# Performance work log

Measured on AMD Instinct MI355X. Metric: run time of the kernel, lower is better.

The kernel has to match this reference:

```python
import jax, jax.numpy as jnp
import numpy as np

H = 8        # n_attention_heads
D = 512      # model_dimension (full per-head dim in this module!)
DFF = 2048   # feed_forward_internal_dimension
B, T = 8, 1024
EPS = 1e-5


def _layernorm(x, g, b, eps=EPS):
    mu = jnp.mean(x, axis=-1, keepdims=True)
    var = jnp.mean(jnp.square(x - mu), axis=-1, keepdims=True)
    return (x - mu) * jax.lax.rsqrt(var + eps) * g + b


def setup_inputs() -> dict:
    key = jax.random.key(0)
    ks = jax.random.split(key, 16)
    s_d = 1.0 / np.sqrt(D)
    s_c = 1.0 / np.sqrt(H * D)
    s_f = 1.0 / np.sqrt(DFF)
    return {
        "x":   jax.random.normal(ks[0], (B, T, D), jnp.float32),
        # per-head projections, stored (in, out); stacked over heads
        "Wq":  jax.random.normal(ks[1], (H, D, D), jnp.float32) * s_d,
        "bq":  jax.random.normal(ks[2], (H, D), jnp.float32) * 0.02,
        "Wk":  jax.random.normal(ks[3], (H, D, D), jnp.float32) * s_d,
        "bk":  jax.random.normal(ks[4], (H, D), jnp.float32) * 0.02,
        "Wv":  jax.random.normal(ks[5], (H, D, D), jnp.float32) * s_d,
        "bv":  jax.random.normal(ks[6], (H, D), jnp.float32) * 0.02,
        "Wo":  jax.random.normal(ks[7], (H * D, D), jnp.float32) * s_c,
        "bo":  jax.random.normal(ks[8], (D,), jnp.float32) * 0.02,
        "ln1_g": 1.0 + 0.1 * jax.random.normal(ks[9], (D,), jnp.float32),
        "ln1_b": 0.1 * jax.random.normal(ks[10], (D,), jnp.float32),
        "W1":  jax.random.normal(ks[11], (D, DFF), jnp.float32) * s_d,
        "b1":  jax.random.normal(ks[12], (DFF,), jnp.float32) * 0.02,
        "W2":  jax.random.normal(ks[13], (DFF, D), jnp.float32) * s_f,
        "b2":  jax.random.normal(ks[14], (D,), jnp.float32) * 0.02,
        "ln2_g": 1.0 + 0.1 * jax.random.normal(ks[15], (D,), jnp.float32),
        "ln2_b": jnp.zeros((D,), jnp.float32),
    }


def reference(x, Wq, bq, Wk, bk, Wv, bv, Wo, bo, ln1_g, ln1_b,
              W1, b1, W2, b2, ln2_g, ln2_b):
    # --- multi-head attention (each head uses the FULL d_model) ---
    # q,k,v: [H, B, T, D]
    q = jnp.einsum("btd,hde->hbte", x, Wq) + bq[:, None, None, :]
    k = jnp.einsum("btd,hde->hbte", x, Wk) + bk[:, None, None, :]
    v = jnp.einsum("btd,hde->hbte", x, Wv) + bv[:, None, None, :]
    scores = jnp.einsum("hbte,hbse->hbts", q, k) * (D ** -0.5)  # [H,B,T,T]
    attn = jax.nn.softmax(scores, axis=-1)
    heads = jnp.einsum("hbts,hbse->hbte", attn, v)  # [H,B,T,D]
    # concat heads along features: [B,T,H*D]
    concat = jnp.transpose(heads, (1, 2, 0, 3)).reshape(x.shape[0], x.shape[1], -1)
    mha = concat @ Wo + bo
    # residual + LayerNorm (dropout_p = 0)
    y1 = _layernorm(mha + x, ln1_g, ln1_b)
    # --- FFN: note source applies ReLU AFTER the second Linear, then skip ---
    ff = jax.nn.relu((y1 @ W1 + b1) @ W2 + b2) + y1
    out = _layernorm(ff, ln2_g, ln2_b)
    return out
```

## Files before the change

kernel.cpp:

```cpp
#include <hip/hip_runtime.h>

using u16 = unsigned short;
using bf16x8 = __attribute__((ext_vector_type(8))) short;
using f32x4 = __attribute__((ext_vector_type(4))) float;

__device__ __forceinline__ u16 f2bf(float f) {
  unsigned x = __float_as_uint(f);
  x += 0x7fffu + ((x >> 16) & 1u);
  return (u16)(x >> 16);
}

__device__ __forceinline__ void gl2lds16(const u16* g, u16* l) {
  __builtin_amdgcn_global_load_lds(
      (const __attribute__((address_space(1))) unsigned int*)g,
      (__attribute__((address_space(3))) unsigned int*)l, 16, 0, 0);
}

__global__ __launch_bounds__(256) void cvt_all(
    const float* __restrict__ x, u16* __restrict__ Krep,
    const float* __restrict__ Wq, const float* __restrict__ Wk,
    const float* __restrict__ Wv, const float* __restrict__ Wo,
    const float* __restrict__ W1, const float* __restrict__ W2,
    u16* __restrict__ Wqb, u16* __restrict__ Wkb, u16* __restrict__ WvT,
    u16* __restrict__ WoT, u16* __restrict__ W1T, u16* __restrict__ W2T)
{
  int b = blockIdx.x, tid = threadIdx.x;
  if (b < 4096) {
    int i = b * 1024 + tid * 4;
    float4 v = *(const float4*)(x + i);
    ushort4 o;
    o.x = f2bf(v.x); o.y = f2bf(v.y); o.z = f2bf(v.z); o.w = f2bf(v.w);
    *(ushort4*)(Krep + i) = o;
    return;
  }
  if (b < 8192) {
    const float* s; u16* d; int i;
    if (b < 6144) { s = Wq; d = Wqb; i = (b - 4096) * 1024 + tid * 4; }
    else          { s = Wk; d = Wkb; i = (b - 6144) * 1024 + tid * 4; }
    float4 v = *(const float4*)(s + i);
    ushort4 o;
    o.x = f2bf(v.x); o.y = f2bf(v.y); o.z = f2bf(v.z); o.w = f2bf(v.w);
    *(ushort4*)(d + i) = o;
    return;
  }
  __shared__ float T[32][33];
  const float* s; u16* d; int K, N, k0, n0;
  int i = b - 8192;
  if (i < 2048) {
    int h = i / 256, tl = i % 256;
    s = Wv + (size_t)h * 262144; d = WvT + (size_t)h * 262144;
    K = 512; N = 512; n0 = (tl % 16) * 32; k0 = (tl / 16) * 32;
  } else if (i < 4096) {
    int j = i - 2048;
    s = Wo; d = WoT; K = 4096; N = 512; n0 = (j % 16) * 32; k0 = (j / 16) * 32;
  } else if (i < 5120) {
    int j = i - 4096;
    s = W1; d = W1T; K = 512; N = 2048; n0 = (j % 64) * 32; k0 = (j / 64) * 32;
  } else {
    int j = i - 5120;
    s = W2; d = W2T; K = 2048; N = 512; n0 = (j % 16) * 32; k0 = (j / 16) * 32;
  }
  int r = tid >> 3, c4 = (tid & 7) << 2;
  float4 v = *(const float4*)(s + (size_t)(k0 + r) * N + n0 + c4);
  T[r][c4 + 0] = v.x; T[r][c4 + 1] = v.y; T[r][c4 + 2] = v.z; T[r][c4 + 3] = v.w;
  __syncthreads();
  ushort4 o;
  o.x = f2bf(T[c4 + 0][r]); o.y = f2bf(T[c4 + 1][r]);
  o.z = f2bf(T[c4 + 2][r]); o.w = f2bf(T[c4 + 3][r]);
  *(ushort4*)(d + (size_t)(n0 + r) * K + k0 + c4) = o;
}

__global__ __launch_bounds__(256) void wk_bias(
    const float* __restrict__ Wk, const float* __restrict__ bq,
    float* __restrict__ wbuf)
{
  int r = blockIdx.x * 4 + (threadIdx.x >> 6);
  int lane = threadIdx.x & 63;
  int h = r >> 9, a = r & 511;
  const float* row = Wk + ((size_t)h * 512 + a) * 512 + lane * 8;
  const float* bqp = bq + h * 512 + lane * 8;
  float4 w0 = *(const float4*)row, w1 = *(const float4*)(row + 4);
  float4 b0 = *(const float4*)bqp, b1 = *(const float4*)(bqp + 4);
  float s = w0.x * b0.x + w0.y * b0.y + w0.z * b0.z + w0.w * b0.w +
            w1.x * b1.x + w1.y * b1.y + w1.z * b1.z + w1.w * b1.w;
  #pragma unroll
  for (int off = 1; off < 64; off <<= 1) s += __shfl_xor(s, off);
  if (lane == 0) wbuf[r] = s;
}

template<int BM>
__global__ __launch_bounds__(256) void gemm_bt(
    const u16* __restrict__ A, const u16* __restrict__ Bt,
    const float* __restrict__ bias, void* __restrict__ Cout,
    int M, int N, int K, int lda, int ldb, long long kzoff,
    long long sBz, long long sbz, long long sCzBytes, int out_mode)
{
  constexpr int MT = BM / 32;
  __shared__ __align__(16) u16 smem[BM * 32 + 128 * 32];
  u16* As = smem;
  u16* Bs = smem + BM * 32;
  const f32x4 zero4 = {0.f, 0.f, 0.f, 0.f};

  const u16* Ap = A + (size_t)blockIdx.z * (size_t)kzoff;
  const u16* Bp = Bt + (size_t)blockIdx.z * (size_t)(sBz + kzoff);
  const float* biasp = bias ? bias + (size_t)blockIdx.z * sbz : nullptr;
  char* Cp = (char*)Cout + (size_t)blockIdx.z * sCzBytes;

  int tid = threadIdx.x;
  int lane = tid & 63, wave = tid >> 6;
  int m = lane & 15, quad = lane >> 4;
  int wm = (wave >> 1) * (BM / 2), wn = (wave & 1) * 64;
  int m0 = blockIdx.y * BM, n0 = blockIdx.x * 128;
  int lr = lane >> 2, lc = (lane & 3) << 3;

  f32x4 acc[MT][4];
  #pragma unroll
  for (int i = 0; i < MT; i++)
    #pragma unroll
    for (int j = 0; j < 4; j++) acc[i][j] = zero4;

  for (int k0 = 0; k0 < K; k0 += 32) {
    #pragma unroll
    for (int i = 0; i < BM / 64; i++) {
      int rb = i * 64 + wave * 16;
      gl2lds16(Ap + (size_t)(m0 + rb + lr) * lda + k0 + lc, &As[rb * 32]);
    }
    #pragma unroll
    for (int i = 0; i < 2; i++) {
      int rb = i * 64 + wave * 16;
      gl2lds16(Bp + (size_t)(n0 + rb + lr) * ldb + k0 + lc, &Bs[rb * 32]);
    }
    __syncthreads();

    bf16x8 af[MT], bfr[4];
    #pragma unroll
    for (int t = 0; t < MT; t++)
      af[t] = *(const bf16x8*)&As[(wm + t * 16 + m) * 32 + quad * 8];
    #pragma unroll
    for (int t = 0; t < 4; t++)
      bfr[t] = *(const bf16x8*)&Bs[(wn + t * 16 + m) * 32 + quad * 8];
    #pragma unroll
    for (int mt = 0; mt < MT; mt++)
      #pragma unroll
      for (int nt = 0; nt < 4; nt++)
        acc[mt][nt] = __builtin_amdgcn_mfma_f32_16x16x32_bf16(af[mt], bfr[nt],
                                                              acc[mt][nt], 0, 0, 0);
    __syncthreads();
  }

  if (out_mode == 2) {
    u16* Ts = smem;
    int b2 = m0 >> 10, t20 = m0 & 1023;
    int half = wave >> 1;
    #pragma unroll
    for (int mt = 0; mt < MT; mt++) {
      #pragma unroll
      for (int nt = 0; nt < 4; nt++) {
        int colc = wn + nt * 16 + m;
        float bb = biasp ? biasp[n0 + colc] : 0.f;
        #pragma unroll
        for (int r = 0; r < 4; r++)
          Ts[colc * 40 + half * 16 + quad * 4 + r] = f2bf(acc[mt][nt][r] + bb);
      }
      __syncthreads();
      #pragma unroll
      for (int it = 0; it < 2; it++) {
        int c = (tid >> 2) + 64 * it;
        int j = tid & 3;
        bf16x8 v = *(const bf16x8*)&Ts[c * 40 + j * 8];
        int tg = t20 + (j >> 1) * (BM / 2) + mt * 16 + (j & 1) * 8;
        *(bf16x8*)((u16*)Cp + ((size_t)b2 * 512 + n0 + c) * 1024 + tg) = v;
      }
      __syncthreads();
    }
    return;
  }

  #pragma unroll
  for (int nt = 0; nt < 4; nt++) {
    int col = n0 + wn + nt * 16 + m;
    float bb = biasp ? biasp[col] : 0.f;
    #pragma unroll
    for (int mt = 0; mt < MT; mt++) {
      #pragma unroll
      for (int r = 0; r < 4; r++) {
        int row = m0 + wm + mt * 16 + quad * 4 + r;
        float v = acc[mt][nt][r] + bb;
        if (out_mode == 1) {
          ((u16*)Cp)[(size_t)row * N + col] = f2bf(v);
        } else {
          ((float*)Cp)[(size_t)row * N + col] = v;
        }
      }
    }
  }
}

__global__ __launch_bounds__(256) void gemm_tv16(
    const u16* __restrict__ A, const u16* __restrict__ Mt,
    const u16* __restrict__ WvT, const float* __restrict__ wbuf,
    const float* __restrict__ bv, u16* __restrict__ Tg, u16* __restrict__ Vg)
{
  __shared__ __align__(16) u16 smem[8192];
  u16* As = smem;
  u16* Bs = smem + 4096;
  const f32x4 zero4 = {0.f, 0.f, 0.f, 0.f};

  int z = blockIdx.z;
  int t = z >> 3, h = z & 7;
  const u16* Bp = (t == 0 ? Mt : WvT) + (size_t)h * 262144;
  const float* biasp = (t == 0 ? wbuf : bv) + h * 512;
  u16* Og = (t == 0 ? Tg : Vg) + (size_t)h * 4194304;

  int tid = threadIdx.x;
  int lane = tid & 63, wave = tid >> 6;
  int m = lane & 15, quad = lane >> 4;
  int wm = (wave >> 1) * 64, wn = (wave & 1) * 64;
  int m0 = blockIdx.y * 128, n0 = blockIdx.x * 128;
  int lr = lane >> 2, lc = (lane & 3) << 3;

  f32x4 acc[4][4];
  #pragma unroll
  for (int i = 0; i < 4; i++)
    #pragma unroll
    for (int j = 0; j < 4; j++) acc[i][j] = zero4;

  for (int k0 = 0; k0 < 512; k0 += 32) {
    #pragma unroll
    for (int i = 0; i < 2; i++) {
      int rb = i * 64 + wave * 16;
      gl2lds16(A + (size_t)(m0 + rb + lr) * 512 + k0 + lc, &As[rb * 32]);
      gl2lds16(Bp + (size_t)(n0 + rb + lr) * 512 + k0 + lc, &Bs[rb * 32]);
    }
    __syncthreads();
    bf16x8 af[4], bfr[4];
    #pragma unroll
    for (int tt = 0; tt < 4; tt++) {
      af[tt]  = *(const bf16x8*)&As[(wm + tt * 16 + m) * 32 + quad * 8];
      bfr[tt] = *(const bf16x8*)&Bs[(wn + tt * 16 + m) * 32 + quad * 8];
    }
    #pragma unroll
    for (int mt = 0; mt < 4; mt++)
      #pragma unroll
      for (int nt = 0; nt < 4; nt++)
        acc[mt][nt] = __builtin_amdgcn_mfma_f32_16x16x32_bf16(af[mt], bfr[nt],
                                                              acc[mt][nt], 0, 0, 0);
    __syncthreads();
  }

  if (t == 1) {
    u16* Ts = smem;
    int b2 = m0 >> 10, t20 = m0 & 1023;
    int half = wave >> 1;
    #pragma unroll
    for (int mt = 0; mt < 4; mt++) {
      #pragma unroll
      for (int nt = 0; nt < 4; nt++) {
        int colc = wn + nt * 16 + m;
        float bb = biasp[n0 + colc];
        #pragma unroll
        for (int r = 0; r < 4; r++)
          Ts[colc * 40 + half * 16 + quad * 4 + r] = f2bf(acc[mt][nt][r] + bb);
      }
      __syncthreads();
      #pragma unroll
      for (int it = 0; it < 2; it++) {
        int c = (tid >> 2) + 64 * it;
        int j = tid & 3;
        bf16x8 v = *(const bf16x8*)&Ts[c * 40 + j * 8];
        int tg = t20 + (j >> 1) * 64 + mt * 16 + (j & 1) * 8;
        *(bf16x8*)(Og + ((size_t)b2 * 512 + n0 + c) * 1024 + tg) = v;
      }
      __syncthreads();
    }
    return;
  }

  #pragma unroll
  for (int nt = 0; nt < 4; nt++) {
    int col = n0 + wn + nt * 16 + m;
    float bb = biasp[col];
    #pragma unroll
    for (int mt = 0; mt < 4; mt++) {
      #pragma unroll
      for (int r = 0; r < 4; r++) {
        int row = m0 + wm + mt * 16 + quad * 4 + r;
        Og[(size_t)row * 512 + col] = f2bf(acc[mt][nt][r] + bb);
      }
    }
  }
}

__global__ __launch_bounds__(256, 2) void attn_kernel(
    const u16* __restrict__ Tg, const u16* __restrict__ Krep,
    const u16* __restrict__ Vg, u16* __restrict__ Oc, int h0)
{
  __shared__ __align__(16) u16 Kt[32][520];
  __shared__ __align__(16) u16 Vt[512][32];
  __shared__ __align__(16) u16 Pl[4][16][40];
  const f32x4 zero4 = {0.f, 0.f, 0.f, 0.f};

  int b = blockIdx.x, qb = blockIdx.y, z = blockIdx.z;
  int h = h0 + z;

  size_t hb = ((size_t)z * 8 + b) * (size_t)(1024 * 512);
  const u16* Tp = Tg + hb;
  const u16* Kp = Krep + (size_t)b * (size_t)(1024 * 512);
  const u16* Vp = Vg + hb;

  int tid = threadIdx.x, lane = tid & 63, wave = tid >> 6;
  int m = lane & 15, quad = lane >> 4;
  int q0 = qb * 64 + wave * 16;

  bf16x8 aq[16];
  #pragma unroll
  for (int kc = 0; kc < 16; kc++)
    aq[kc] = *(const bf16x8*)(Tp + (size_t)(q0 + m) * 512 + kc * 32 + quad * 8);

  f32x4 acc[32];
  #pragma unroll
  for (int dt = 0; dt < 32; dt++) acc[dt] = zero4;
  f32x4 lsum = zero4;
  const float scale = 0.04419417382415922f;
  short one = 0x3F80;
  bf16x8 bones = {one, one, one, one, one, one, one, one};

  int vrow = lane >> 2;
  int vcol = (lane & 3) << 3;

  for (int kt = 0; kt < 32; kt++) {
    int kr0 = kt * 32;
    #pragma unroll
    for (int r = 0; r < 8; r++) {
      int row = wave * 8 + r;
      gl2lds16(Kp + (size_t)(kr0 + row) * 512 + lane * 8, &Kt[row][0]);
    }
    #pragma unroll
    for (int i = 0; i < 8; i++) {
      int j = wave * 8 + i;
      gl2lds16(Vp + (size_t)(j * 16 + vrow) * 1024 + kr0 + vcol, &Vt[j * 16][0]);
    }
    __syncthreads();

    f32x4 s0 = zero4, s1 = zero4;
    __builtin_amdgcn_s_setprio(1);
    #pragma unroll
    for (int kc = 0; kc < 16; kc++) {
      bf16x8 bk0 = *(const bf16x8*)&Kt[m][kc * 32 + quad * 8];
      bf16x8 bk1 = *(const bf16x8*)&Kt[m + 16][kc * 32 + quad * 8];
      s0 = __builtin_amdgcn_mfma_f32_16x16x32_bf16(aq[kc], bk0, s0, 0, 0, 0);
      s1 = __builtin_amdgcn_mfma_f32_16x16x32_bf16(aq[kc], bk1, s1, 0, 0, 0);
    }
    __builtin_amdgcn_s_setprio(0);

    #pragma unroll
    for (int r = 0; r < 4; r++) {
      Pl[wave][quad * 4 + r][m]      = f2bf(__expf(s0[r] * scale));
      Pl[wave][quad * 4 + r][m + 16] = f2bf(__expf(s1[r] * scale));
    }
    asm volatile("s_waitcnt lgkmcnt(0)" ::: "memory");
    bf16x8 ap = *(const bf16x8*)&Pl[wave][m][quad * 8];

    lsum = __builtin_amdgcn_mfma_f32_16x16x32_bf16(ap, bones, lsum, 0, 0, 0);

    __builtin_amdgcn_s_setprio(1);
    #pragma unroll
    for (int dt = 0; dt < 32; dt++) {
      bf16x8 bv = *(const bf16x8*)&Vt[dt * 16 + m][quad * 8];
      acc[dt] = __builtin_amdgcn_mfma_f32_16x16x32_bf16(ap, bv, acc[dt], 0, 0, 0);
    }
    __builtin_amdgcn_s_setprio(0);
    __syncthreads();
  }

  float linv[4];
  #pragma unroll
  for (int r = 0; r < 4; r++) linv[r] = 1.f / lsum[r];
  #pragma unroll
  for (int dt = 0; dt < 32; dt++) {
    #pragma unroll
    for (int r = 0; r < 4; r++) {
      size_t trow = (size_t)b * 1024 + q0 + quad * 4 + r;
      Oc[(trow * 8 + h) * 512 + dt * 16 + m] = f2bf(acc[dt][r] * linv[r]);
    }
  }
}

__global__ __launch_bounds__(256) void ln_kernel(
    const float* __restrict__ xin0, const float* __restrict__ xin1,
    const float* __restrict__ bias, const float* __restrict__ res,
    const float* __restrict__ gam, const float* __restrict__ bet,
    float* __restrict__ outf, u16* __restrict__ outb, int do_relu)
{
  __shared__ float red[4];
  __shared__ float red2[4];
  int row = blockIdx.x, t = threadIdx.x;
  size_t base = (size_t)row * 512;
  float a0 = xin0[base + t] + bias[t];
  float a1 = xin0[base + 256 + t] + bias[256 + t];
  if (xin1) { a0 += xin1[base + t]; a1 += xin1[base + 256 + t]; }
  if (do_relu) { a0 = fmaxf(a0, 0.f); a1 = fmaxf(a1, 0.f); }
  a0 += res[base + t]; a1 += res[base + 256 + t];

  float s = a0 + a1;
  #pragma unroll
  for (int off = 32; off > 0; off >>= 1) s += __shfl_xor(s, off);
  if ((t & 63) == 0) red[t >> 6] = s;
  __syncthreads();
  float mu = (red[0] + red[1] + red[2] + red[3]) * (1.f / 512.f);

  float d0 = a0 - mu, d1 = a1 - mu;
  float q = d0 * d0 + d1 * d1;
  #pragma unroll
  for (int off = 32; off > 0; off >>= 1) q += __shfl_xor(q, off);
  if ((t & 63) == 0) red2[t >> 6] = q;
  __syncthreads();
  float var = (red2[0] + red2[1] + red2[2] + red2[3]) * (1.f / 512.f);
  float rs = rsqrtf(var + 1e-5f);

  float o0 = d0 * rs * gam[t] + bet[t];
  float o1 = d1 * rs * gam[t + 256] + bet[t + 256];
  outf[base + t] = o0;
  outf[base + 256 + t] = o1;
  if (outb) { outb[base + t] = f2bf(o0); outb[base + 256 + t] = f2bf(o1); }
}

extern "C" void kernel_launch(void* const* d_in, const int* in_sizes, int n_in,
                              void* d_out, int out_size, void* d_ws, size_t ws_size,
                              hipStream_t stream) {
  const float* x   = (const float*)d_in[0];
  const float* Wq  = (const float*)d_in[1];
  const float* bq  = (const float*)d_in[2];
  const float* Wk  = (const float*)d_in[3];
  const float* bk  = (const float*)d_in[4];
  const float* Wv  = (const float*)d_in[5];
  const float* bv  = (const float*)d_in[6];
  const float* Wo  = (const float*)d_in[7];
  const float* bo  = (const float*)d_in[8];
  const float* g1  = (const float*)d_in[9];
  const float* bn1 = (const float*)d_in[10];
  const float* W1  = (const float*)d_in[11];
  const float* bf1 = (const float*)d_in[12];
  const float* W2  = (const float*)d_in[13];
  const float* bf2 = (const float*)d_in[14];
  const float* g2  = (const float*)d_in[15];
  const float* bn2 = (const float*)d_in[16];
  (void)bk;

  const size_t HB = 8388608;
  char* ws = (char*)d_ws;
  u16* Krep = (u16*)(ws + 0);
  u16* xb   = Krep;
  u16* Wqb = (u16*)(ws + 67108864);
  u16* Wkb = (u16*)(ws + 71303168);
  u16* WvT = (u16*)(ws + 75497472);
  u16* WoT = (u16*)(ws + 79691776);
  u16* W1T = (u16*)(ws + 83886080);
  u16* W2T = (u16*)(ws + 85983232);
  u16* Mt  = (u16*)(ws + 88080384);
  float* wbuf = (float*)(ws + 92274688);
  u16* cc  = (u16*)(ws + 92291072);
  size_t tvbase = 159399936;
  size_t G = 1;
  if (ws_size >= 293617664ULL) G = 8;
  else if (ws_size >= 226508800ULL) G = 4;
  else if (ws_size >= 218120192ULL) G = 2;
  u16* Tg = (u16*)(ws + tvbase);
  u16* Vg = (u16*)(ws + tvbase + G * HB);
  float* y1f  = (float*)(ws + 159399936);
  u16*   y1b  = (u16*)(ws + 176177152);
  float* mha0 = (float*)(ws + 184565760);
  float* mha1 = (float*)(ws + 201342976);
  u16*   ff1  = (u16*)(ws + 92291072);
  float* ff20 = (float*)(ws + 125845504);
  float* ff21 = (float*)(ws + 142622720);

  cvt_all<<<14336, 256, 0, stream>>>(x, Krep, Wq, Wk, Wv, Wo, W1, W2,
                                     Wqb, Wkb, WvT, WoT, W1T, W2T);
  gemm_bt<128><<<dim3(4, 4, 8), 256, 0, stream>>>(Wkb, Wqb, nullptr, Mt,
      512, 512, 512, 512, 512, 262144LL, 0LL, 0LL, 524288LL, 1);
  wk_bias<<<1024, 256, 0, stream>>>(Wk, bq, wbuf);

  dim3 blk(256);
  if (G == 8) {
    gemm_tv16<<<dim3(4, 64, 16), blk, 0, stream>>>(xb, Mt, WvT, wbuf, bv,
                                                   Tg, Vg);
    attn_kernel<<<dim3(8, 16, 8), 256, 0, stream>>>(Tg, Krep, Vg, cc, 0);
  } else {
    for (int h0 = 0; h0 < 8; h0 += (int)G) {
      dim3 gqkv(4, 64, (unsigned)G);
      gemm_bt<128><<<gqkv, blk, 0, stream>>>(xb, Mt + (size_t)h0 * 262144,
          wbuf + h0 * 512, Tg, 8192, 512, 512, 512, 512, 0LL,
          262144LL, 512LL, (long long)HB, 1);
      gemm_bt<128><<<gqkv, blk, 0, stream>>>(xb, WvT + (size_t)h0 * 262144,
          bv + h0 * 512, Vg, 8192, 512, 512, 512, 512, 0LL,
          262144LL, 512LL, (long long)HB, 2);
      attn_kernel<<<dim3(8, 16, (unsigned)G), 256, 0, stream>>>(Tg, Krep, Vg,
                                                                cc, h0);
    }
  }

  gemm_bt<64><<<dim3(4, 128, 2), blk, 0, stream>>>(cc, WoT, nullptr, mha0,
      8192, 512, 2048, 4096, 4096, 2048LL, 0LL, 0LL, 16777216LL, 0);
  ln_kernel<<<8192, 256, 0, stream>>>(mha0, mha1, bo, x, g1, bn1, y1f, y1b, 0);

  gemm_bt<128><<<dim3(16, 64, 1), blk, 0, stream>>>(y1b, W1T, bf1, ff1,
      8192, 2048, 512, 512, 512, 0LL, 0LL, 0LL, 0LL, 1);

  gemm_bt<64><<<dim3(4, 128, 2), blk, 0, stream>>>(ff1, W2T, nullptr, ff20,
      8192, 512, 1024, 2048, 2048, 1024LL, 0LL, 0LL, 16777216LL, 0);

  ln_kernel<<<8192, 256, 0, stream>>>(ff20, ff21, bf2, y1f, g2, bn2,
                                      (float*)d_out, nullptr, 1);
}
```

Measured before the change: 664.9 us.

## Restructure attention PV into 32x32 MFMA tiles with prefetched K/V and swizzled LDS

Reworks the attention kernel's P·V stage to use 32x32x16 MFMA tiles, with waves split across query halves and D halves instead of per-wave 16-row tiles. K and V for the next key tile are prefetched into LDS right after the buffers are consumed, using split barriers and vmcnt waits to overlap global loads with compute. The V tile uses an XOR-swizzled LDS layout to avoid bank conflicts. The row-sum MFMA against a ones vector is replaced by shuffle reductions on the rounded P values. The risk is that a single K/V buffer and more barriers per iteration may limit overlap, and the LDS and register footprint changes.

```diff
diff --git a/kernel.cpp b/kernel.cpp
--- a/kernel.cpp
+++ b/kernel.cpp
@@ -3,6 +3,7 @@
 using u16 = unsigned short;
 using bf16x8 = __attribute__((ext_vector_type(8))) short;
 using f32x4 = __attribute__((ext_vector_type(4))) float;
+using f32x16 = __attribute__((ext_vector_type(16))) float;
 
 __device__ __forceinline__ u16 f2bf(float f) {
   unsigned x = __float_as_uint(f);
@@ -296,9 +297,12 @@
     const u16* __restrict__ Vg, u16* __restrict__ Oc, int h0)
 {
   __shared__ __align__(16) u16 Kt[32][520];
-  __shared__ __align__(16) u16 Vt[512][32];
-  __shared__ __align__(16) u16 Pl[4][16][40];
+  __shared__ __align__(16) u16 Vt[512 * 32];
+  __shared__ __align__(16) u16 Pl[64][40];
+  __shared__ float lred[64];
   const f32x4 zero4 = {0.f, 0.f, 0.f, 0.f};
+  const f32x16 zero16 = {0.f,0.f,0.f,0.f,0.f,0.f,0.f,0.f,
+                         0.f,0.f,0.f,0.f,0.f,0.f,0.f,0.f};
 
   int b = blockIdx.x, qb = blockIdx.y, z = blockIdx.z;
   int h = h0 + z;
@@ -310,40 +314,43 @@
 
   int tid = threadIdx.x, lane = tid & 63, wave = tid >> 6;
   int m = lane & 15, quad = lane >> 4;
+  int l31 = lane & 31, hi = lane >> 5;
+  int qh = wave >> 1, dh = wave & 1;
   int q0 = qb * 64 + wave * 16;
+
+  int vr = lane >> 2;
+  int vc = (((lane & 3) ^ ((lane >> 3) & 3)) << 3);
+  int vswz = (l31 >> 1) & 3;
 
   bf16x8 aq[16];
   #pragma unroll
   for (int kc = 0; kc < 16; kc++)
     aq[kc] = *(const bf16x8*)(Tp + (size_t)(q0 + m) * 512 + kc * 32 + quad * 8);
 
-  f32x4 acc[32];
-  #pragma unroll
-  for (int dt = 0; dt < 32; dt++) acc[dt] = zero4;
-  f32x4 lsum = zero4;
+  f32x16 o[8];
+  #pragma unroll
+  for (int dt = 0; dt < 8; dt++) o[dt] = zero16;
+  float lsum_acc[4] = {0.f, 0.f, 0.f, 0.f};
   const float scale = 0.04419417382415922f;
-  short one = 0x3F80;
-  bf16x8 bones = {one, one, one, one, one, one, one, one};
-
-  int vrow = lane >> 2;
-  int vcol = (lane & 3) << 3;
+
+  #pragma unroll
+  for (int r = 0; r < 8; r++) {
+    int row = wave * 8 + r;
+    gl2lds16(Kp + (size_t)row * 512 + lane * 8, &Kt[row][0]);
+  }
+  #pragma unroll
+  for (int j = 0; j < 8; j++) {
+    int rb = wave * 128 + j * 16;
+    gl2lds16(Vp + (size_t)(rb + vr) * 1024 + vc, &Vt[rb * 32]);
+  }
 
   for (int kt = 0; kt < 32; kt++) {
-    int kr0 = kt * 32;
-    #pragma unroll
-    for (int r = 0; r < 8; r++) {
-      int row = wave * 8 + r;
-      gl2lds16(Kp + (size_t)(kr0 + row) * 512 + lane * 8, &Kt[row][0]);
-    }
-    #pragma unroll
-    for (int i = 0; i < 8; i++) {
-      int j = wave * 8 + i;
-      gl2lds16(Vp + (size_t)(j * 16 + vrow) * 1024 + kr0 + vcol, &Vt[j * 16][0]);
-    }
-    __syncthreads();
+    asm volatile("s_waitcnt vmcnt(8)" ::: "memory");
+    __builtin_amdgcn_sched_barrier(0);
+    __builtin_amdgcn_s_barrier();
+    __builtin_amdgcn_sched_barrier(0);
 
     f32x4 s0 = zero4, s1 = zero4;
-    __builtin_amdgcn_s_setprio(1);
     #pragma unroll
     for (int kc = 0; kc < 16; kc++) {
       bf16x8 bk0 = *(const bf16x8*)&Kt[m][kc * 32 + quad * 8];
@@ -351,37 +358,87 @@
       s0 = __builtin_amdgcn_mfma_f32_16x16x32_bf16(aq[kc], bk0, s0, 0, 0, 0);
       s1 = __builtin_amdgcn_mfma_f32_16x16x32_bf16(aq[kc], bk1, s1, 0, 0, 0);
     }
-    __builtin_amdgcn_s_setprio(0);
 
     #pragma unroll
     for (int r = 0; r < 4; r++) {
-      Pl[wave][quad * 4 + r][m]      = f2bf(__expf(s0[r] * scale));
-      Pl[wave][quad * 4 + r][m + 16] = f2bf(__expf(s1[r] * scale));
-    }
+      float e0 = __expf(s0[r] * scale);
+      float e1 = __expf(s1[r] * scale);
+      u16 p0 = f2bf(e0), p1 = f2bf(e1);
+      int prow = wave * 16 + quad * 4 + r;
+      Pl[prow][m] = p0;
+      Pl[prow][m + 16] = p1;
+      float t = __uint_as_float((unsigned)p0 << 16) +
+                __uint_as_float((unsigned)p1 << 16);
+      t += __shfl_xor(t, 1); t += __shfl_xor(t, 2);
+      t += __shfl_xor(t, 4); t += __shfl_xor(t, 8);
+      lsum_acc[r] += t;
+    }
+
+    asm volatile("s_waitcnt vmcnt(0) lgkmcnt(0)" ::: "memory");
+    __builtin_amdgcn_sched_barrier(0);
+    __builtin_amdgcn_s_barrier();
+    __builtin_amdgcn_sched_barrier(0);
+
+    if (kt < 31) {
+      int kr1 = (kt + 1) * 32;
+      #pragma unroll
+      for (int r = 0; r < 8; r++) {
+        int row = wave * 8 + r;
+        gl2lds16(Kp + (size_t)(kr1 + row) * 512 + lane * 8, &Kt[row][0]);
+      }
+    }
+
+    const u16* PlRow = &Pl[qh * 32 + l31][0];
+    #pragma unroll
+    for (int ks = 0; ks < 2; ks++) {
+      bf16x8 pa = *(const bf16x8*)(PlRow + ks * 16 + hi * 8);
+      #pragma unroll
+      for (int dt = 0; dt < 8; dt++) {
+        int rr = dh * 256 + dt * 32 + l31;
+        int cc2 = (((ks * 2 + hi) ^ vswz) << 3);
+        bf16x8 bv = *(const bf16x8*)&Vt[rr * 32 + cc2];
+        o[dt] = __builtin_amdgcn_mfma_f32_32x32x16_bf16(pa, bv, o[dt], 0, 0, 0);
+      }
+    }
+
     asm volatile("s_waitcnt lgkmcnt(0)" ::: "memory");
-    bf16x8 ap = *(const bf16x8*)&Pl[wave][m][quad * 8];
-
-    lsum = __builtin_amdgcn_mfma_f32_16x16x32_bf16(ap, bones, lsum, 0, 0, 0);
-
-    __builtin_amdgcn_s_setprio(1);
-    #pragma unroll
-    for (int dt = 0; dt < 32; dt++) {
-      bf16x8 bv = *(const bf16x8*)&Vt[dt * 16 + m][quad * 8];
-      acc[dt] = __builtin_amdgcn_mfma_f32_16x16x32_bf16(ap, bv, acc[dt], 0, 0, 0);
-    }
-    __builtin_amdgcn_s_setprio(0);
-    __syncthreads();
-  }
-
-  float linv[4];
-  #pragma unroll
-  for (int r = 0; r < 4; r++) linv[r] = 1.f / lsum[r];
-  #pragma unroll
-  for (int dt = 0; dt < 32; dt++) {
-    #pragma unroll
-    for (int r = 0; r < 4; r++) {
-      size_t trow = (size_t)b * 1024 + q0 + quad * 4 + r;
-      Oc[(trow * 8 + h) * 512 + dt * 16 + m] = f2bf(acc[dt][r] * linv[r]);
+    __builtin_amdgcn_sched_barrier(0);
+    __builtin_amdgcn_s_barrier();
+    __builtin_amdgcn_sched_barrier(0);
+
+    if (kt < 31) {
+      int kr1 = (kt + 1) * 32;
+      #pragma unroll
+      for (int j = 0; j < 8; j++) {
+        int rb = wave * 128 + j * 16;
+        gl2lds16(Vp + (size_t)(rb + vr) * 1024 + kr1 + vc, &Vt[rb * 32]);
+      }
+    }
+  }
+
+  if (m == 0) {
+    #pragma unroll
+    for (int r = 0; r < 4; r++)
+      lred[wave * 16 + quad * 4 + r] = lsum_acc[r];
+  }
+  __syncthreads();
+
+  float linv[16];
+  #pragma unroll
+  for (int g = 0; g < 4; g++) {
+    float4 t = *(const float4*)&lred[qh * 32 + 8 * g + 4 * hi];
+    linv[4 * g + 0] = 1.f / t.x; linv[4 * g + 1] = 1.f / t.y;
+    linv[4 * g + 2] = 1.f / t.z; linv[4 * g + 3] = 1.f / t.w;
+  }
+
+  size_t obase = (size_t)b * 1024 + qb * 64 + qh * 32;
+  #pragma unroll
+  for (int dt = 0; dt < 8; dt++) {
+    int dcol = dh * 256 + dt * 32 + l31;
+    #pragma unroll
+    for (int reg = 0; reg < 16; reg++) {
+      int rowq = (reg & 3) + 8 * (reg >> 2) + 4 * hi;
+      Oc[((obase + rowq) * 8 + h) * 512 + dcol] = f2bf(o[dt][reg] * linv[reg]);
     }
   }
 }
```

Measured after the change: 661.5 us. Within noise of the previous version (-0.5%).
